# Kernel optimization log

Hardware: AMD Instinct MI355X
Metric: run time of the kernel (lower is better)

Reference implementation:

```python
import jax, jax.numpy as jnp
import numpy as np

DIM = 1024
HEADS = 16
DIM_HEAD = 64
SCALE = DIM_HEAD ** -0.5
LN_EPS = 1e-5


def layer_norm(x, g, b):
    mu = jnp.mean(x, axis=-1, keepdims=True)
    var = jnp.mean(jnp.square(x - mu), axis=-1, keepdims=True)
    return (x - mu) * jax.lax.rsqrt(var + LN_EPS) * g + b


def setup_inputs() -> dict:
    key = jax.random.key(0)
    ks = jax.random.split(key, 8)
    w_std = DIM ** -0.5  # keep GEMM outputs O(1)
    return {
        "query": jax.random.normal(ks[0], (4, 512, DIM), jnp.float32),
        "kv": jax.random.normal(ks[1], (4, 2048, DIM), jnp.float32),
        "ln_q_g": jnp.ones((DIM,), jnp.float32),
        "ln_q_b": jnp.zeros((DIM,), jnp.float32),
        "ln_kv_g": jnp.ones((DIM,), jnp.float32),
        "ln_kv_b": jnp.zeros((DIM,), jnp.float32),
        "Wq": jax.random.normal(ks[2], (DIM, DIM), jnp.float32) * w_std,
        "bq": jnp.zeros((DIM,), jnp.float32),
        "Wk": jax.random.normal(ks[3], (DIM, DIM), jnp.float32) * w_std,
        "bk": jnp.zeros((DIM,), jnp.float32),
        "Wv": jax.random.normal(ks[4], (DIM, DIM), jnp.float32) * w_std,
        "bv": jnp.zeros((DIM,), jnp.float32),
        "Wo": jax.random.normal(ks[5], (DIM, DIM), jnp.float32) * w_std,
        "bo": jnp.zeros((DIM,), jnp.float32),
    }


def reference(query, kv, ln_q_g, ln_q_b, ln_kv_g, ln_kv_b,
              Wq, bq, Wk, bk, Wv, bv, Wo, bo):
    kv_n = layer_norm(kv, ln_kv_g, ln_kv_b)            # (b, n_kv, d)
    residual = query
    q_n = layer_norm(query, ln_q_g, ln_q_b)            # (b, n_q, d)

    q = q_n @ Wq + bq                                   # (b, n_q, inner)
    kv_input = jnp.concatenate((kv_n, q_n), axis=-2)    # (b, n_kv+n_q, d)
    k = kv_input @ Wk + bk
    v = kv_input @ Wv + bv

    def split_heads(t):
        b, n, _ = t.shape
        return t.reshape(b, n, HEADS, DIM_HEAD).transpose(0, 2, 1, 3)  # b h n dh

    q = split_heads(q) * SCALE
    k = split_heads(k)
    v = split_heads(v)

    sim = jnp.einsum('bhid,bhjd->bhij', q, k)           # (b, h, n_q, n_kv+n_q)
    sim = sim - jax.lax.stop_gradient(jnp.max(sim, axis=-1, keepdims=True))
    attn = jax.nn.softmax(sim, axis=-1)
    out = jnp.einsum('bhij,bhjd->bhid', attn, v)        # (b, h, n_q, dh)

    b, h, n, dh = out.shape
    out = out.transpose(0, 2, 1, 3).reshape(b, n, h * dh)
    return out @ Wo + bo + residual
```

## Files before the change

### kernel.cpp

```cpp
#include <hip/hip_runtime.h>
#include <hip/hip_bf16.h>

#define B_    4
#define NQ    512
#define NKV   2048
#define NT    2560
#define DIM_  1024
#define HEADS 16
#define DH    64
#define NSEQT 10240
#define SCALE_Q_L2E 0.18033688011112042f

typedef short bf16x8 __attribute__((ext_vector_type(8)));
typedef float f32x4  __attribute__((ext_vector_type(4)));
typedef __hip_bfloat16 bf16;

__device__ inline void gll16(const bf16* g, bf16* l) {
  __builtin_amdgcn_global_load_lds(
      (const __attribute__((address_space(1))) unsigned int*)g,
      (__attribute__((address_space(3))) unsigned int*)l, 16, 0, 0);
}

#define SBAR() do { __builtin_amdgcn_s_barrier(); __builtin_amdgcn_sched_barrier(0); } while (0)
#define VMCNT(n) asm volatile("s_waitcnt vmcnt(" #n ")" ::: "memory")

__global__ __launch_bounds__(256) void prep_kernel(
    const float* __restrict__ query, const float* __restrict__ kv,
    const float* __restrict__ lgq, const float* __restrict__ lbq,
    const float* __restrict__ lgkv, const float* __restrict__ lbkv,
    bf16* __restrict__ X,
    const float* __restrict__ W0, const float* __restrict__ W1,
    const float* __restrict__ W2, const float* __restrict__ W3,
    bf16* __restrict__ T0, bf16* __restrict__ T1,
    bf16* __restrict__ T2, bf16* __restrict__ T3)
{
  __shared__ __align__(16) char psm[9216];
  const int t = threadIdx.x;
  const int blkid = blockIdx.x;
  if (blkid < B_*NT) {
    float* sh = (float*)psm;
    int b = blkid / NT, r = blkid % NT;
    const float *src, *g, *bb;
    if (r < NKV) { src = kv    + ((size_t)b*NKV + r)*DIM_;      g = lgkv; bb = lbkv; }
    else         { src = query + ((size_t)b*NQ + (r-NKV))*DIM_; g = lgq;  bb = lbq;  }
    float4 v = ((const float4*)src)[t];
    float s  = v.x+v.y+v.z+v.w;
    float s2 = v.x*v.x+v.y*v.y+v.z*v.z+v.w*v.w;
    #pragma unroll
    for (int m=1;m<64;m<<=1){ s += __shfl_xor(s,m,64); s2 += __shfl_xor(s2,m,64); }
    int wave=t>>6, lane=t&63;
    if(lane==0){ sh[wave]=s; sh[4+wave]=s2; }
    __syncthreads();
    s  = sh[0]+sh[1]+sh[2]+sh[3];
    s2 = sh[4]+sh[5]+sh[6]+sh[7];
    float mu = s*(1.0f/DIM_);
    float rs = rsqrtf(s2*(1.0f/DIM_) - mu*mu + 1e-5f);
    float4 gg = ((const float4*)g)[t];
    float4 b4 = ((const float4*)bb)[t];
    bf16* dst = X + (size_t)blkid*DIM_ + t*4;
    dst[0]=__float2bfloat16((v.x-mu)*rs*gg.x + b4.x);
    dst[1]=__float2bfloat16((v.y-mu)*rs*gg.y + b4.y);
    dst[2]=__float2bfloat16((v.z-mu)*rs*gg.z + b4.z);
    dst[3]=__float2bfloat16((v.w-mu)*rs*gg.w + b4.w);
  } else {
    int l = blkid - B_*NT;
    const float* W; bf16* Wt;
    switch (l>>8) {
      case 0: W=W0; Wt=T0; break;
      case 1: W=W1; Wt=T1; break;
      case 2: W=W2; Wt=T2; break;
      default: W=W3; Wt=T3; break;
    }
    int rem = l & 255;
    int k0 = (rem&15)*64, n0 = (rem>>4)*64;
    bf16* Ws = (bf16*)psm;
    int kr = t>>2, nseg = (t&3)*16;
    const float4* s4 = (const float4*)(W + (size_t)(k0+kr)*DIM_ + n0 + nseg);
    union { uint4 u[2]; bf16 h[16]; } pk;
    #pragma unroll
    for (int j=0;j<4;j++){
      float4 v = s4[j];
      pk.h[j*4+0]=__float2bfloat16(v.x); pk.h[j*4+1]=__float2bfloat16(v.y);
      pk.h[j*4+2]=__float2bfloat16(v.z); pk.h[j*4+3]=__float2bfloat16(v.w);
    }
    *(uint4*)(Ws + kr*72 + nseg)     = pk.u[0];
    *(uint4*)(Ws + kr*72 + nseg + 8) = pk.u[1];
    __syncthreads();
    int n = t&63, kseg = t>>6;
    union { uint4 u[2]; bf16 h[16]; } o;
    #pragma unroll
    for (int k=0;k<16;k++) o.h[k] = Ws[(kseg*16+k)*72 + n];
    bf16* dst = Wt + (size_t)(n0+n)*DIM_ + k0 + kseg*16;
    *(uint4*)dst = o.u[0];
    *(uint4*)(dst+8) = o.u[1];
  }
}

__device__ __forceinline__ void gemm_core(
    const bf16* __restrict__ A, const bf16* __restrict__ Bmat,
    const float* __restrict__ bias, const float* __restrict__ residual,
    void* __restrict__ outv, int rows_per_batch, int row_offset,
    int a_batch_stride_rows, int n_seq, float scale,
    int emode, int m0, int n0, char* smem)
{
  bf16* As = (bf16*)smem;
  bf16* Bs = (bf16*)(smem + 8192);
  float* Ts = (float*)smem;

  const int t = threadIdx.x;
  const int r0 = t>>2, c8 = (t&3)*8;
  int gm0 = m0 + r0, gm1 = m0 + 64 + r0;
  int b0i = gm0 / rows_per_batch, b1i = gm1 / rows_per_batch;
  const bf16* a0 = A + ((size_t)b0i*a_batch_stride_rows + row_offset + (gm0 - b0i*rows_per_batch))*(size_t)DIM_ + c8;
  const bf16* a1 = A + ((size_t)b1i*a_batch_stride_rows + row_offset + (gm1 - b1i*rows_per_batch))*(size_t)DIM_ + c8;
  const bf16* wb0 = Bmat + (size_t)(n0 + r0)*DIM_ + c8;
  const bf16* wb1 = Bmat + (size_t)(n0 + 64 + r0)*DIM_ + c8;
  bf16* lA0 = As + t*8;  bf16* lA1 = As + 64*32 + t*8;
  bf16* lB0 = Bs + t*8;  bf16* lB1 = Bs + 64*32 + t*8;

  const int wave = t>>6, lane = t&63, qq = lane>>4, mr = lane&15;
  const int wm = (wave>>1)*64, wn = (wave&1)*64;

  f32x4 acc[4][4] = {};
  for (int k0 = 0; k0 < DIM_; k0 += 32) {
    gll16(a0 + k0, lA0);
    gll16(a1 + k0, lA1);
    gll16(wb0 + k0, lB0);
    gll16(wb1 + k0, lB1);
    __syncthreads();
    bf16x8 af[4], bfr[4];
    #pragma unroll
    for (int ms=0;ms<4;ms++) af[ms]  = *(const bf16x8*)(As + (wm+ms*16+mr)*32 + qq*8);
    #pragma unroll
    for (int ns=0;ns<4;ns++) bfr[ns] = *(const bf16x8*)(Bs + (wn+ns*16+mr)*32 + qq*8);
    #pragma unroll
    for (int ms=0;ms<4;ms++)
      #pragma unroll
      for (int ns=0;ns<4;ns++)
        acc[ms][ns] = __builtin_amdgcn_mfma_f32_16x16x32_bf16(af[ms], bfr[ns], acc[ms][ns], 0,0,0);
    __syncthreads();
  }

  const int lr = t>>3, cs = (t&7)*16;
  for (int R=0; R<4; R++){
    if ((wave>>1) == (R>>1)) {
      #pragma unroll
      for (int ms2=0; ms2<2; ms2++){
        int ms = (R&1)*2 + ms2;
        #pragma unroll
        for (int ns=0; ns<4; ns++){
          int col = wn + ns*16 + mr;
          #pragma unroll
          for (int r=0;r<4;r++)
            Ts[(ms2*16 + qq*4 + r)*132 + col] = acc[ms][ns][r];
        }
      }
    }
    __syncthreads();
    float v[16];
    #pragma unroll
    for (int j=0;j<4;j++){
      float4 f = *(const float4*)(Ts + lr*132 + cs + j*4);
      v[j*4+0]=f.x; v[j*4+1]=f.y; v[j*4+2]=f.z; v[j*4+3]=f.w;
    }
    int gr = m0 + R*32 + lr;
    int gc = n0 + cs;
    if (emode == 0) {
      float* out = (float*)outv;
      size_t base = (size_t)gr*DIM_ + gc;
      #pragma unroll
      for (int j=0;j<4;j++){
        float4 bv = *(const float4*)(bias + gc + j*4);
        float4 rv = *(const float4*)(residual + base + j*4);
        float4 o4;
        o4.x = v[j*4+0] + bv.x + rv.x;
        o4.y = v[j*4+1] + bv.y + rv.y;
        o4.z = v[j*4+2] + bv.z + rv.z;
        o4.w = v[j*4+3] + bv.w + rv.w;
        *(float4*)(out + base + j*4) = o4;
      }
    } else if (emode == 1) {
      int bb = gr / rows_per_batch;
      int n  = gr - bb*rows_per_batch;
      int hh = gc>>6, dh = gc&63;
      bf16* out = (bf16*)outv + ((size_t)(bb*HEADS + hh)*n_seq + n)*DH + dh;
      union { uint4 u[2]; bf16 h[16]; } pk;
      #pragma unroll
      for (int j=0;j<16;j++) pk.h[j] = __float2bfloat16((v[j] + bias[gc+j])*scale);
      *(uint4*)out     = pk.u[0];
      *(uint4*)(out+8) = pk.u[1];
    } else {
      float bc = bias[gr];
      bf16* out = (bf16*)outv + (size_t)gr*NSEQT + gc;
      union { uint4 u[2]; bf16 h[16]; } pk;
      #pragma unroll
      for (int j=0;j<16;j++) pk.h[j] = __float2bfloat16(v[j] + bc);
      *(uint4*)out     = pk.u[0];
      *(uint4*)(out+8) = pk.u[1];
    }
    __syncthreads();
  }
}

#define MFMA8(mbase, nbase, BF)                                               \
  do {                                                                        \
    __builtin_amdgcn_s_setprio(1);                                            \
    _Pragma("unroll")                                                         \
    for (int ms = 0; ms < 4; ++ms)                                            \
      _Pragma("unroll")                                                       \
      for (int ns = 0; ns < 2; ++ns) {                                        \
        acc[(mbase)+ms][(nbase)+ns] = __builtin_amdgcn_mfma_f32_16x16x32_bf16(\
            af[ms][0], BF[ns][0], acc[(mbase)+ms][(nbase)+ns], 0,0,0);        \
        acc[(mbase)+ms][(nbase)+ns] = __builtin_amdgcn_mfma_f32_16x16x32_bf16(\
            af[ms][1], BF[ns][1], acc[(mbase)+ms][(nbase)+ns], 0,0,0);        \
      }                                                                       \
    __builtin_amdgcn_s_setprio(0);                                            \
  } while (0)

__global__ __launch_bounds__(512, 2) void gemm_qkv2(
    const bf16* __restrict__ X,
    const bf16* __restrict__ WtQ, const bf16* __restrict__ WtK,
    const bf16* __restrict__ WtV,
    const float* __restrict__ bq, const float* __restrict__ bk,
    const float* __restrict__ bv,
    bf16* __restrict__ Qhb, bf16* __restrict__ Khb, bf16* __restrict__ VTg)
{
  __shared__ __align__(16) char smem[131072];
  const int t   = threadIdx.x;
  const int blk = blockIdx.x;

  const bf16 *A, *Bm; const float* bias; bf16* outp;
  int m0, n0, amode, emode, npb, nseq; float scale;
  if (blk < 32) {
    A = X; Bm = WtQ; bias = bq; outp = Qhb;
    m0 = (blk & 7) * 256; n0 = (blk >> 3) * 256;
    amode = 1; emode = 1; npb = NQ; nseq = NQ; scale = SCALE_Q_L2E;
  } else if (blk < 192) {
    int l = blk - 32;
    A = X; Bm = WtK; bias = bk; outp = Khb;
    m0 = (l % 40) * 256; n0 = (l / 40) * 256;
    amode = 0; emode = 1; npb = NT; nseq = NT; scale = 1.0f;
  } else {
    int l = blk - 192;
    A = WtV; Bm = X; bias = bv; outp = VTg;
    m0 = (l / 40) * 256; n0 = (l % 40) * 256;
    amode = 0; emode = 2; npb = DIM_; nseq = 1; scale = 1.0f;
  }

  const int srow = t >> 3;
  const int gsw  = (t & 7) ^ (srow & 7);
  const bf16* pA[4]; const bf16* pB[4];
  #pragma unroll
  for (int c = 0; c < 4; ++c) {
    int gm = m0 + c*64 + srow;
    int sr = amode ? ((gm >> 9) * NT + NKV + (gm & (NQ-1))) : gm;
    pA[c] = A  + (size_t)sr * DIM_ + gsw * 8;
    pB[c] = Bm + (size_t)(n0 + c*64 + srow) * DIM_ + gsw * 8;
  }

  const int wave = t >> 6, lane = t & 63;
  const int qq = lane >> 4, mr = lane & 15;
  const int wr = wave >> 2, wc = wave & 3;
  const int xg0 = ( qq      ^ (mr & 7)) << 4;
  const int xg1 = ((4 + qq) ^ (mr & 7)) << 4;
  const int awb = (wr*128 + mr) * 128;
  const int bwb = (wc*64  + mr) * 128;
  char* const sA = smem;
  char* const sB = smem + 65536;
  const int toff = t * 16;

  f32x4 acc[8][4] = {};

  gll16(pB[0], (bf16*)(sB + 0*8192 + toff));
  gll16(pB[1], (bf16*)(sB + 1*8192 + toff));
  gll16(pB[2], (bf16*)(sB + 2*8192 + toff));
  gll16(pB[3], (bf16*)(sB + 3*8192 + toff));
  gll16(pA[0], (bf16*)(sA + 0*8192 + toff));
  gll16(pA[2], (bf16*)(sA + 2*8192 + toff));
  gll16(pA[1], (bf16*)(sA + 1*8192 + toff));
  gll16(pA[3], (bf16*)(sA + 3*8192 + toff));
  VMCNT(2);
  SBAR();

  for (int kt = 0; kt < 16; ++kt) {
    char* AsB = sA + ((kt & 1) << 15);
    char* BsB = sB + ((kt & 1) << 15);
    char* AsN = sA + (((kt + 1) & 1) << 15);
    char* BsN = sB + (((kt + 1) & 1) << 15);
    const int kn = ((kt + 1) & 15) << 6;

    bf16x8 af[4][2], bf0[2][2], bf1[2][2];

    #pragma unroll
    for (int ms = 0; ms < 4; ++ms) {
      af[ms][0] = *(const bf16x8*)(AsB + awb + ms*2048 + xg0);
      af[ms][1] = *(const bf16x8*)(AsB + awb + ms*2048 + xg1);
    }
    #pragma unroll
    for (int ns = 0; ns < 2; ++ns) {
      bf0[ns][0] = *(const bf16x8*)(BsB + bwb + ns*2048 + xg0);
      bf0[ns][1] = *(const bf16x8*)(BsB + bwb + ns*2048 + xg1);
    }
    gll16(pB[0] + kn, (bf16*)(BsN + 0*8192 + toff));
    gll16(pB[1] + kn, (bf16*)(BsN + 1*8192 + toff));
    SBAR();
    MFMA8(0, 0, bf0);
    SBAR();

    #pragma unroll
    for (int ns = 0; ns < 2; ++ns) {
      bf1[ns][0] = *(const bf16x8*)(BsB + bwb + (2+ns)*2048 + xg0);
      bf1[ns][1] = *(const bf16x8*)(BsB + bwb + (2+ns)*2048 + xg1);
    }
    gll16(pB[2] + kn, (bf16*)(BsN + 2*8192 + toff));
    gll16(pB[3] + kn, (bf16*)(BsN + 3*8192 + toff));
    SBAR();
    MFMA8(0, 2, bf1);
    VMCNT(4);
    SBAR();

    #pragma unroll
    for (int ms = 0; ms < 4; ++ms) {
      af[ms][0] = *(const bf16x8*)(AsB + awb + (4+ms)*2048 + xg0);
      af[ms][1] = *(const bf16x8*)(AsB + awb + (4+ms)*2048 + xg1);
    }
    gll16(pA[0] + kn, (bf16*)(AsN + 0*8192 + toff));
    gll16(pA[2] + kn, (bf16*)(AsN + 2*8192 + toff));
    SBAR();
    MFMA8(4, 0, bf0);
    SBAR();

    gll16(pA[1] + kn, (bf16*)(AsN + 1*8192 + toff));
    gll16(pA[3] + kn, (bf16*)(AsN + 3*8192 + toff));
    SBAR();
    MFMA8(4, 2, bf1);
    VMCNT(2);
    SBAR();
  }

  VMCNT(0);
  __syncthreads();

  float* Of = (float*)smem;
  const int er = t >> 4, ec = (t & 15) * 16;
  #pragma unroll
  for (int R = 0; R < 8; ++R) {
    if (wr == (R >> 2)) {
      #pragma unroll
      for (int j = 0; j < 2; ++j)
        #pragma unroll
        for (int nf = 0; nf < 4; ++nf)
          #pragma unroll
          for (int r = 0; r < 4; ++r)
            Of[(j*16 + qq*4 + r)*264 + wc*64 + nf*16 + mr] = acc[((R&3)<<1)+j][nf][r];
    }
    __syncthreads();
    {
      int gr = m0 + R*32 + er;
      int gc = n0 + ec;
      float v[16];
      #pragma unroll
      for (int j = 0; j < 4; ++j) {
        float4 f = *(const float4*)(Of + er*264 + ec + j*4);
        v[j*4+0]=f.x; v[j*4+1]=f.y; v[j*4+2]=f.z; v[j*4+3]=f.w;
      }
      if (emode == 1) {
        int bb = gr / npb, n = gr - bb*npb;
        int hh = gc >> 6, dh = gc & 63;
        bf16* o = outp + ((size_t)(bb*HEADS + hh)*nseq + n)*DH + dh;
        union { uint4 u[2]; bf16 h[16]; } pk;
        #pragma unroll
        for (int j = 0; j < 16; ++j) pk.h[j] = __float2bfloat16((v[j] + bias[gc+j])*scale);
        *(uint4*)o     = pk.u[0];
        *(uint4*)(o+8) = pk.u[1];
      } else {
        float bc = bias[gr];
        bf16* o = outp + (size_t)gr*NSEQT + gc;
        union { uint4 u[2]; bf16 h[16]; } pk;
        #pragma unroll
        for (int j = 0; j < 16; ++j) pk.h[j] = __float2bfloat16(v[j] + bc);
        *(uint4*)o     = pk.u[0];
        *(uint4*)(o+8) = pk.u[1];
      }
    }
    __syncthreads();
  }
}

__global__ __launch_bounds__(256) void gemm_o(
    const bf16* __restrict__ Ctx, const bf16* __restrict__ WtO,
    const float* __restrict__ bo, const float* __restrict__ residual,
    float* __restrict__ out)
{
  __shared__ __align__(16) char smem[16896];
  const int blk = blockIdx.x;
  gemm_core(Ctx, WtO, bo, residual, out, B_*NQ, 0, B_*NQ, NQ, 1.0f, 0,
            (blk&15)*128, (blk>>4)*128, smem);
}

__global__ __launch_bounds__(256) void attn6_kernel(
    const bf16* __restrict__ Qh, const bf16* __restrict__ Kh,
    const bf16* __restrict__ VTg, bf16* __restrict__ Ctx)
{
  __shared__ __align__(16) bf16 KV[2][8192];
  __shared__ __align__(16) unsigned int Ps[4][640];

  const int t = threadIdx.x, wave = t>>6, lane = t&63;
  const int qq = lane>>4, mr = lane&15;
  const int blk = blockIdx.x;
  const int bh = (blk&7)*8 + (blk>>6);
  const int q0 = ((blk>>3)&7)*64;
  const int b = bh>>4, h = bh&15;
  const int pair = wave>>1, kh = wave&1;
  const int qb = pair*32;

  const int sl = t>>2, sc = t&3;
  const int skey = 32*(sl>>5) + 2*(sl&15) + ((sl>>4)&1);
  const bf16* Kb  = Kh + (size_t)bh*NT*DH + (size_t)skey*DH + sc*8;
  const bf16* VbT = VTg + ((size_t)(h*DH) + sl)*NSEQT + (size_t)b*NT + sc*8;

  bf16x8 qf[2][2];
  #pragma unroll
  for (int mt=0; mt<2; mt++){
    const bf16* Qb = Qh + ((size_t)bh*NQ + q0 + qb + mt*16 + mr)*DH;
    qf[mt][0] = *(const bf16x8*)(Qb + qq*8);
    qf[mt][1] = *(const bf16x8*)(Qb + 32 + qq*8);
  }

  f32x4 o[2][4] = {};
  float l[2][4] = {};
  unsigned int* Pw = &Ps[wave][0];

  {
    bf16* bp = &KV[0][0];
    gll16(Kb,        bp + t*8);
    gll16(Kb + 32,   bp + 2048 + t*8);
    gll16(VbT,       bp + 4096 + t*8);
    gll16(VbT + 32,  bp + 6144 + t*8);
  }

  for (int it = 0; it < NT/64; it++) {
    __syncthreads();
    if (it + 1 < NT/64) {
      int kt = (it+1)*64;
      bf16* bp = &KV[(it+1)&1][0];
      gll16(Kb  + (size_t)kt*DH,      bp + t*8);
      gll16(Kb  + (size_t)kt*DH + 32, bp + 2048 + t*8);
      gll16(VbT + kt,                 bp + 4096 + t*8);
      gll16(VbT + kt + 32,            bp + 6144 + t*8);
    }
    const bf16* cbuf = &KV[it&1][0];

    bf16x8 kf[2][2];
    #pragma unroll
    for (int g=0; g<2; g++){
      kf[g][0] = *(const bf16x8*)(cbuf + (32*kh + 16*g + mr)*32 + qq*8);
      kf[g][1] = *(const bf16x8*)(cbuf + 2048 + (32*kh + 16*g + mr)*32 + qq*8);
    }
    f32x4 s[2][2];
    #pragma unroll
    for (int mt=0; mt<2; mt++)
      #pragma unroll
      for (int g=0; g<2; g++){
        f32x4 z = {};
        z = __builtin_amdgcn_mfma_f32_16x16x32_bf16(qf[mt][0], kf[g][0], z, 0,0,0);
        z = __builtin_amdgcn_mfma_f32_16x16x32_bf16(qf[mt][1], kf[g][1], z, 0,0,0);
        s[mt][g] = z;
      }
    bf16x8 vf[4];
    #pragma unroll
    for (int n2=0; n2<4; n2++)
      vf[n2] = *(const bf16x8*)(cbuf + 4096 + kh*2048 + (n2*16+mr)*32 + qq*8);

    #pragma unroll
    for (int mt=0; mt<2; mt++)
      #pragma unroll
      for (int r=0; r<4; r++){
        float e0 = __builtin_amdgcn_exp2f(s[mt][0][r]);
        float e1 = __builtin_amdgcn_exp2f(s[mt][1][r]);
        l[mt][r] += e0 + e1;
        unsigned a0 = __float_as_uint(e0) + 0x8000u;
        unsigned a1 = __float_as_uint(e1) + 0x8000u;
        Pw[(mt*16 + qq*4 + r)*20 + mr] = __builtin_amdgcn_perm(a1, a0, 0x07060302u);
      }
    asm volatile("s_waitcnt lgkmcnt(0)" ::: "memory");
    bf16x8 pa[2];
    #pragma unroll
    for (int mt=0; mt<2; mt++)
      pa[mt] = *(const bf16x8*)(Pw + (mt*16+mr)*20 + qq*4);
    #pragma unroll
    for (int mt=0; mt<2; mt++)
      #pragma unroll
      for (int n2=0; n2<4; n2++)
        o[mt][n2] = __builtin_amdgcn_mfma_f32_16x16x32_bf16(pa[mt], vf[n2], o[mt][n2], 0,0,0);
  }

  float lsum[2][4];
  #pragma unroll
  for (int mt=0; mt<2; mt++)
    #pragma unroll
    for (int r=0; r<4; r++){
      float v = l[mt][r];
      #pragma unroll
      for (int m=1;m<16;m<<=1) v += __shfl_xor(v, m, 16);
      lsum[mt][r] = v;
    }

  __syncthreads();
  float* Of  = (float*)&KV[0][0];
  float* lsh = (float*)&Ps[0][0];
  if (kh == 1) {
    #pragma unroll
    for (int mt=0; mt<2; mt++){
      #pragma unroll
      for (int n2=0; n2<4; n2++)
        #pragma unroll
        for (int r=0; r<4; r++)
          Of[(qb + mt*16 + qq*4 + r)*68 + n2*16 + mr] = o[mt][n2][r];
      if (mr == 0)
        #pragma unroll
        for (int r=0; r<4; r++)
          lsh[qb + mt*16 + qq*4 + r] = lsum[mt][r];
    }
  }
  __syncthreads();
  if (kh == 0) {
    #pragma unroll
    for (int mt=0; mt<2; mt++)
      #pragma unroll
      for (int r=0; r<4; r++){
        int row = qb + mt*16 + qq*4 + r;
        float rl = 1.0f / (lsum[mt][r] + lsh[row]);
        #pragma unroll
        for (int n2=0; n2<4; n2++){
          int idx = row*68 + n2*16 + mr;
          Of[idx] = (o[mt][n2][r] + Of[idx]) * rl;
        }
      }
  }
  __syncthreads();
  {
    int row = t>>2, seg = (t&3)*16;
    union { uint4 u[2]; bf16 hh[16]; } pkv;
    #pragma unroll
    for (int j=0;j<16;j++) pkv.hh[j] = __float2bfloat16(Of[row*68 + seg + j]);
    bf16* dst = Ctx + ((size_t)b*NQ + q0 + row)*DIM_ + h*DH + seg;
    *(uint4*)dst = pkv.u[0];
    *(uint4*)(dst+8) = pkv.u[1];
  }
}

extern "C" void kernel_launch(void* const* d_in, const int* in_sizes, int n_in,
                              void* d_out, int out_size, void* d_ws, size_t ws_size,
                              hipStream_t stream)
{
  const float* query  = (const float*)d_in[0];
  const float* kv     = (const float*)d_in[1];
  const float* ln_q_g = (const float*)d_in[2];
  const float* ln_q_b = (const float*)d_in[3];
  const float* ln_kv_g= (const float*)d_in[4];
  const float* ln_kv_b= (const float*)d_in[5];
  const float* Wq = (const float*)d_in[6];
  const float* bq = (const float*)d_in[7];
  const float* Wk = (const float*)d_in[8];
  const float* bk = (const float*)d_in[9];
  const float* Wv = (const float*)d_in[10];
  const float* bv = (const float*)d_in[11];
  const float* Wo = (const float*)d_in[12];
  const float* bo = (const float*)d_in[13];
  float* out = (float*)d_out;

  char* ws = (char*)d_ws;
  size_t off = 0;
  auto take = [&](size_t bytes)->char* {
    char* p = ws + off; off += (bytes + 255) & ~(size_t)255; return p;
  };
  bf16* X    = (bf16*)take((size_t)B_*NT*DIM_*2);
  bf16* Qhb  = (bf16*)take((size_t)B_*NQ*DIM_*2);
  bf16* Khb  = (bf16*)take((size_t)B_*NT*DIM_*2);
  bf16* VTg  = (bf16*)take((size_t)DIM_*NSEQT*2);
  bf16* Ctx  = (bf16*)take((size_t)B_*NQ*DIM_*2);
  bf16* WtQ  = (bf16*)take((size_t)DIM_*DIM_*2);
  bf16* WtK  = (bf16*)take((size_t)DIM_*DIM_*2);
  bf16* WtV  = (bf16*)take((size_t)DIM_*DIM_*2);
  bf16* WtO  = (bf16*)take((size_t)DIM_*DIM_*2);

  prep_kernel<<<B_*NT + 1024, 256, 0, stream>>>(
      query, kv, ln_q_g, ln_q_b, ln_kv_g, ln_kv_b, X,
      Wq, Wk, Wv, Wo, WtQ, WtK, WtV, WtO);

  gemm_qkv2<<<352, 512, 0, stream>>>(X, WtQ, WtK, WtV, bq, bk, bv,
                                     Qhb, Khb, VTg);

  attn6_kernel<<<512, 256, 0, stream>>>(Qhb, Khb, VTg, Ctx);

  gemm_o<<<128, 256, 0, stream>>>(Ctx, WtO, bo, query, out);
}
```

Measured before the change: 270.9 us.

## Restructure QKV GEMM main loop into k-half phases with unrolled double buffering

Rewrites the QKV projection GEMM inner loop so each 64-wide k-tile is processed in two 32-wide halves across four phases. Each phase loads 4 A and 4 B fragments and issues 16 MFMAs, replacing the old split of A into two row halves with 2-wide k fragments. The loop is unrolled by two to alternate LDS buffers statically, and global-to-LDS stage loads are spread across the phases. The sched_barrier after each barrier is dropped and vmcnt waits go to zero, which trades fewer live fragment registers and static buffer addressing for possibly less overlap of loads and a different compiler schedule.

```diff
diff --git a/kernel.cpp b/kernel.cpp
--- a/kernel.cpp
+++ b/kernel.cpp
@@ -21,8 +21,8 @@
       (__attribute__((address_space(3))) unsigned int*)l, 16, 0, 0);
 }
 
-#define SBAR() do { __builtin_amdgcn_s_barrier(); __builtin_amdgcn_sched_barrier(0); } while (0)
 #define VMCNT(n) asm volatile("s_waitcnt vmcnt(" #n ")" ::: "memory")
+#define BAR() __builtin_amdgcn_s_barrier()
 
 __global__ __launch_bounds__(256) void prep_kernel(
     const float* __restrict__ query, const float* __restrict__ kv,
@@ -202,21 +202,6 @@
   }
 }
 
-#define MFMA8(mbase, nbase, BF)                                               \
-  do {                                                                        \
-    __builtin_amdgcn_s_setprio(1);                                            \
-    _Pragma("unroll")                                                         \
-    for (int ms = 0; ms < 4; ++ms)                                            \
-      _Pragma("unroll")                                                       \
-      for (int ns = 0; ns < 2; ++ns) {                                        \
-        acc[(mbase)+ms][(nbase)+ns] = __builtin_amdgcn_mfma_f32_16x16x32_bf16(\
-            af[ms][0], BF[ns][0], acc[(mbase)+ms][(nbase)+ns], 0,0,0);        \
-        acc[(mbase)+ms][(nbase)+ns] = __builtin_amdgcn_mfma_f32_16x16x32_bf16(\
-            af[ms][1], BF[ns][1], acc[(mbase)+ms][(nbase)+ns], 0,0,0);        \
-      }                                                                       \
-    __builtin_amdgcn_s_setprio(0);                                            \
-  } while (0)
-
 __global__ __launch_bounds__(512, 2) void gemm_qkv2(
     const bf16* __restrict__ X,
     const bf16* __restrict__ WtQ, const bf16* __restrict__ WtK,
@@ -271,72 +256,74 @@
 
   f32x4 acc[8][4] = {};
 
-  gll16(pB[0], (bf16*)(sB + 0*8192 + toff));
-  gll16(pB[1], (bf16*)(sB + 1*8192 + toff));
-  gll16(pB[2], (bf16*)(sB + 2*8192 + toff));
-  gll16(pB[3], (bf16*)(sB + 3*8192 + toff));
-  gll16(pA[0], (bf16*)(sA + 0*8192 + toff));
-  gll16(pA[2], (bf16*)(sA + 2*8192 + toff));
-  gll16(pA[1], (bf16*)(sA + 1*8192 + toff));
-  gll16(pA[3], (bf16*)(sA + 3*8192 + toff));
-  VMCNT(2);
-  SBAR();
-
-  for (int kt = 0; kt < 16; ++kt) {
-    char* AsB = sA + ((kt & 1) << 15);
-    char* BsB = sB + ((kt & 1) << 15);
-    char* AsN = sA + (((kt + 1) & 1) << 15);
-    char* BsN = sB + (((kt + 1) & 1) << 15);
-    const int kn = ((kt + 1) & 15) << 6;
-
-    bf16x8 af[4][2], bf0[2][2], bf1[2][2];
-
-    #pragma unroll
-    for (int ms = 0; ms < 4; ++ms) {
-      af[ms][0] = *(const bf16x8*)(AsB + awb + ms*2048 + xg0);
-      af[ms][1] = *(const bf16x8*)(AsB + awb + ms*2048 + xg1);
-    }
-    #pragma unroll
-    for (int ns = 0; ns < 2; ++ns) {
-      bf0[ns][0] = *(const bf16x8*)(BsB + bwb + ns*2048 + xg0);
-      bf0[ns][1] = *(const bf16x8*)(BsB + bwb + ns*2048 + xg1);
-    }
-    gll16(pB[0] + kn, (bf16*)(BsN + 0*8192 + toff));
-    gll16(pB[1] + kn, (bf16*)(BsN + 1*8192 + toff));
-    SBAR();
-    MFMA8(0, 0, bf0);
-    SBAR();
-
-    #pragma unroll
-    for (int ns = 0; ns < 2; ++ns) {
-      bf1[ns][0] = *(const bf16x8*)(BsB + bwb + (2+ns)*2048 + xg0);
-      bf1[ns][1] = *(const bf16x8*)(BsB + bwb + (2+ns)*2048 + xg1);
-    }
-    gll16(pB[2] + kn, (bf16*)(BsN + 2*8192 + toff));
-    gll16(pB[3] + kn, (bf16*)(BsN + 3*8192 + toff));
-    SBAR();
-    MFMA8(0, 2, bf1);
-    VMCNT(4);
-    SBAR();
-
-    #pragma unroll
-    for (int ms = 0; ms < 4; ++ms) {
-      af[ms][0] = *(const bf16x8*)(AsB + awb + (4+ms)*2048 + xg0);
-      af[ms][1] = *(const bf16x8*)(AsB + awb + (4+ms)*2048 + xg1);
-    }
-    gll16(pA[0] + kn, (bf16*)(AsN + 0*8192 + toff));
-    gll16(pA[2] + kn, (bf16*)(AsN + 2*8192 + toff));
-    SBAR();
-    MFMA8(4, 0, bf0);
-    SBAR();
-
-    gll16(pA[1] + kn, (bf16*)(AsN + 1*8192 + toff));
-    gll16(pA[3] + kn, (bf16*)(AsN + 3*8192 + toff));
-    SBAR();
-    MFMA8(4, 2, bf1);
-    VMCNT(2);
-    SBAR();
-  }
+#define ARD(ABASE, MH, XG)                                                    \
+  do { _Pragma("unroll")                                                      \
+    for (int ms = 0; ms < 4; ++ms)                                            \
+      af[ms] = *(const bf16x8*)((ABASE) + awb + (MH)*8192 + ms*2048 + (XG));  \
+  } while (0)
+#define BRD(BBASE, XG)                                                        \
+  do { _Pragma("unroll")                                                      \
+    for (int n = 0; n < 4; ++n)                                               \
+      bfc[n] = *(const bf16x8*)((BBASE) + bwb + n*2048 + (XG));               \
+  } while (0)
+#define MM(MH)                                                                \
+  do {                                                                        \
+    __builtin_amdgcn_s_setprio(1);                                            \
+    _Pragma("unroll")                                                         \
+    for (int ms = 0; ms < 4; ++ms)                                            \
+      _Pragma("unroll")                                                       \
+      for (int n = 0; n < 4; ++n)                                             \
+        acc[(MH)*4+ms][n] = __builtin_amdgcn_mfma_f32_16x16x32_bf16(          \
+            af[ms], bfc[n], acc[(MH)*4+ms][n], 0,0,0);                        \
+    __builtin_amdgcn_s_setprio(0);                                            \
+  } while (0)
+#define STGA(DST, C, KO) gll16(pA[C] + (KO), (bf16*)((DST) + (C)*8192 + toff))
+#define STGB(DST, C, KO) gll16(pB[C] + (KO), (bf16*)((DST) + (C)*8192 + toff))
+
+  STGA(sA, 0, 0); STGA(sA, 1, 0); STGA(sA, 2, 0); STGA(sA, 3, 0);
+  STGB(sB, 0, 0); STGB(sB, 1, 0); STGB(sB, 2, 0); STGB(sB, 3, 0);
+  VMCNT(0);
+  BAR();
+
+  for (int j = 0; j < 8; ++j) {
+    const int ko1 = (2*j + 1) << 6;
+    const int ko2 = ((2*j + 2) & 15) << 6;
+    bf16x8 af[4], bfc[4];
+
+    ARD(sA, 0, xg0); BRD(sB, xg0);
+    STGA(sA + 32768, 0, ko1); STGA(sA + 32768, 1, ko1);
+    STGB(sB + 32768, 0, ko1); STGB(sB + 32768, 1, ko1);
+    BAR(); MM(0); BAR();
+    ARD(sA, 1, xg0);
+    STGA(sA + 32768, 2, ko1); STGA(sA + 32768, 3, ko1);
+    STGB(sB + 32768, 2, ko1); STGB(sB + 32768, 3, ko1);
+    BAR(); MM(1); BAR();
+    ARD(sA, 0, xg1); BRD(sB, xg1);
+    BAR(); MM(0); BAR();
+    ARD(sA, 1, xg1);
+    VMCNT(0);
+    BAR(); MM(1); BAR();
+
+    ARD(sA + 32768, 0, xg0); BRD(sB + 32768, xg0);
+    STGA(sA, 0, ko2); STGA(sA, 1, ko2);
+    STGB(sB, 0, ko2); STGB(sB, 1, ko2);
+    BAR(); MM(0); BAR();
+    ARD(sA + 32768, 1, xg0);
+    STGA(sA, 2, ko2); STGA(sA, 3, ko2);
+    STGB(sB, 2, ko2); STGB(sB, 3, ko2);
+    BAR(); MM(1); BAR();
+    ARD(sA + 32768, 0, xg1); BRD(sB + 32768, xg1);
+    BAR(); MM(0); BAR();
+    ARD(sA + 32768, 1, xg1);
+    VMCNT(0);
+    BAR(); MM(1); BAR();
+  }
+
+#undef ARD
+#undef BRD
+#undef MM
+#undef STGA
+#undef STGB
 
   VMCNT(0);
   __syncthreads();
```

New measurement: 273.5 us. Within noise of the previous version (+1.0%).
